# Kernel tuning notes

Measured on AMD Instinct MI355X. Metric: run time of the kernel, lower is better.

The kernel has to match this reference:

```python
import jax, jax.numpy as jnp
import numpy as np

NEG_SLOPE = 0.1
BN_EPS = 1e-5

def lrelu(z):
    return jax.nn.leaky_relu(z, NEG_SLOPE)

def conv1d(x, w, b):
    # x: [B,C,L], w: [O,I,K], 'same' padding for K=3
    y = jax.lax.conv_general_dilated(x, w, (1,), [(1, 1)], dimension_numbers=('NCH', 'OIH', 'NCH'))
    return y + b[None, :, None]

def batchnorm_train(x, g, be):
    # training-mode BatchNorm1d over (B, L) per channel; x: [B,C,L]
    m = x.mean(axis=(0, 2), keepdims=True)
    v = x.var(axis=(0, 2), keepdims=True)
    return g[None, :, None] * (x - m) * jax.lax.rsqrt(v + BN_EPS) + be[None, :, None]

def setup_inputs() -> dict:
    key = jax.random.key(0)
    ks = jax.random.split(key, 16)
    L, B, E = 100, 32, 512
    F, K, M, H, DEC = 256, 3, 128, 512, 512
    D = F + 2  # cnn feats + 2 coord dims
    s = 0.02
    inp = {
        'x': jax.random.normal(ks[0], (L, B, E), jnp.float32),
        'h': jax.random.normal(ks[1], (B, H), jnp.float32),
        'cw1': jax.random.normal(ks[2], (F, E, K), jnp.float32) * s,
        'cb1': jnp.zeros((F,), jnp.float32),
        'g1': jnp.ones((F,), jnp.float32), 'be1': jnp.zeros((F,), jnp.float32),
        'cw2': jax.random.normal(ks[3], (F, F, K), jnp.float32) * s,
        'cb2': jnp.zeros((F,), jnp.float32),
        'g2': jnp.ones((F,), jnp.float32), 'be2': jnp.zeros((F,), jnp.float32),
        'cw3': jax.random.normal(ks[4], (F, F, K), jnp.float32) * s,
        'cb3': jnp.zeros((F,), jnp.float32),
        'g3': jnp.ones((F,), jnp.float32), 'be3': jnp.zeros((F,), jnp.float32),
        'cw4': jax.random.normal(ks[5], (F, F, K), jnp.float32) * s,
        'cb4': jnp.zeros((F,), jnp.float32),
        'g4': jnp.ones((F,), jnp.float32), 'be4': jnp.zeros((F,), jnp.float32),
        'W1': jax.random.normal(ks[6], (2 * D + H, M), jnp.float32) * s,
        'b1': jnp.zeros((M,), jnp.float32),
        'W2': jax.random.normal(ks[7], (M, M), jnp.float32) * s,
        'b2': jnp.zeros((M,), jnp.float32),
        'W3': jax.random.normal(ks[8], (M, M), jnp.float32) * s,
        'b3': jnp.zeros((M,), jnp.float32),
        'W4': jax.random.normal(ks[9], (M, M), jnp.float32) * s,
        'b4': jnp.zeros((M,), jnp.float32),
        'F1': jax.random.normal(ks[10], (M, M), jnp.float32) * s,
        'fb1': jnp.zeros((M,), jnp.float32),
        'F2': jax.random.normal(ks[11], (M, DEC), jnp.float32) * s,
        'fb2': jnp.zeros((DEC,), jnp.float32),
    }
    return inp

def reference(x, h, cw1, cb1, g1, be1, cw2, cb2, g2, be2, cw3, cb3, g3, be3,
              cw4, cb4, g4, be4, W1, b1, W2, b2, W3, b3, W4, b4, F1, fb1, F2, fb2):
    # x: [L,B,E] -> [B,E,L]
    xc = jnp.transpose(x, (1, 2, 0))
    for cw, cb, g, be in ((cw1, cb1, g1, be1), (cw2, cb2, g2, be2),
                          (cw3, cb3, g3, be3), (cw4, cb4, g4, be4)):
        xc = batchnorm_train(lrelu(conv1d(xc, cw, cb)), g, be)
    xc = jnp.transpose(xc, (0, 2, 1))  # [B,L,F]
    B, L, _ = xc.shape
    # coordinate tensor: cvt_coord(i, L) = [(i/sqrt(L)-2)/2, (i%sqrt(L)-2)/2]
    i = jnp.arange(L, dtype=jnp.float32)
    sL = jnp.sqrt(jnp.float32(L))
    coord = jnp.stack([(i / sL - 2.0) / 2.0, (jnp.mod(i, sL) - 2.0) / 2.0], axis=-1)
    xf = jnp.concatenate([xc, jnp.broadcast_to(coord, (B, L, 2))], axis=-1)  # [B,L,D]
    D = xf.shape[-1]
    # pair[b,i,j] = [xf[b,j], xf[b,i], h[b]]; split W1 to avoid materializing concat
    Wa, Wb, Wc = W1[:D], W1[D:2 * D], W1[2 * D:]
    A = xf @ Wa                              # contribution of x_j, [B,L,M]
    C = xf @ Wb + (h @ Wc + b1)[:, None, :]  # contribution of x_i and h, [B,L,M]
    g = lrelu(C[:, :, None, :] + A[:, None, :, :])  # [B,L,L,M]
    g = lrelu(g @ W2 + b2)
    g = lrelu(g @ W3 + b3)
    g = lrelu(g @ W4 + b4)
    s = g.sum(axis=(1, 2))  # sum-pool over all L*L pairs -> [B,M]
    out = lrelu(lrelu(s @ F1 + fb1) @ F2 + fb2)  # [B,dec_hid]
    return out
```

## Files before the change

### kernel.cpp

```cpp
#include <hip/hip_runtime.h>
#include <hip/hip_bf16.h>
#include <stdint.h>
#include <stddef.h>

#define NEG 0.1f

typedef __attribute__((ext_vector_type(8))) short short8;
typedef __attribute__((ext_vector_type(16))) float floatx16;

__device__ __forceinline__ unsigned f2bf(float f) {
  union { float f; unsigned u; } v; v.f = f;
  unsigned r = v.u + 0x7FFFu + ((v.u >> 16) & 1u);
  return r >> 16;
}
__device__ __forceinline__ unsigned pk2bf(float a, float b) {
  __hip_bfloat162 h = __float22bfloat162_rn(make_float2(a, b));
  union { __hip_bfloat162 h; unsigned u; } v; v.h = h; return v.u;
}
__device__ __forceinline__ float bits2f(unsigned u) {
  union { unsigned u; float f; } v; v.u = u; return v.f;
}

__global__ void k_prep(const float* __restrict__ cw1, const float* __restrict__ cw2,
                       const float* __restrict__ cw3, const float* __restrict__ cw4,
                       unsigned short* __restrict__ wt1, unsigned short* __restrict__ wt2,
                       unsigned short* __restrict__ wt3, unsigned short* __restrict__ wt4,
                       const float* __restrict__ W1, unsigned short* __restrict__ wab,
                       const float* __restrict__ W2, const float* __restrict__ W3,
                       const float* __restrict__ W4, unsigned short* __restrict__ wmlp,
                       const float* __restrict__ h, float* __restrict__ hc) {
  __shared__ float tile[64 * 65];
  int bid = blockIdx.x, tid = threadIdx.x;
  if (bid < 1280) {
    int z = bid;
    int E; const float* cw; unsigned short* wt;
    if (z < 512) { E = 512; cw = cw1; wt = wt1; }
    else {
      int q = (z - 512) >> 8; E = 256;
      cw = (q == 0) ? cw2 : ((q == 1) ? cw3 : cw4);
      wt = (q == 0) ? wt2 : ((q == 1) ? wt3 : wt4);
      z = (z - 512) & 255;
    }
    int idx = z * 256 + tid;
    int f = idx / E, e = idx - f * E;
    const float* s = cw + (size_t)idx * 3;
    unsigned short* d = wt + (size_t)f * 3 * E + e;
    d[0] = (unsigned short)f2bf(s[0]);
    d[E] = (unsigned short)f2bf(s[1]);
    d[2 * E] = (unsigned short)f2bf(s[2]);
  } else if (bid < 1304) {
    int tw = bid - 1280;
    int half = tw / 12, rem = tw % 12, dt = rem >> 1, nt = rem & 1;
    int c = tid & 63, rq = tid >> 6;
#pragma unroll
    for (int it = 0; it < 16; ++it) {
      int r = rq + it * 4;
      int kp = dt * 64 + r;
      float v = 0.f;
      if (kp < 258) v = W1[(size_t)(half * 258 + kp) * 128 + nt * 64 + c];
      tile[r * 65 + c] = v;
    }
    __syncthreads();
#pragma unroll
    for (int it = 0; it < 16; ++it) {
      int r2 = rq + it * 4;
      wab[(size_t)(half * 128 + nt * 64 + r2) * 384 + dt * 64 + c] =
          (unsigned short)f2bf(tile[c * 65 + r2]);
    }
  } else if (bid < 1496) {
    int i2 = (bid - 1304) * 256 + tid;
    int n = i2 & 127, k = (i2 >> 7) & 127, zz = i2 >> 14;
    const float* W = (zz == 0) ? W2 : ((zz == 1) ? W3 : W4);
    float v = W[k * 128 + n];
    int w = n >> 5, l = ((k >> 3) & 1) * 32 + (n & 31), kk = k >> 4, j = k & 7;
    int i = (((zz * 4 + w) * 8 + kk) << 9) | (l << 3) | j;
    wmlp[i] = (unsigned short)f2bf(v);
  } else {
    int t = bid - 1496;
    int b = t >> 2, seg = t & 3;
    int m = tid & 127, sub = tid >> 7;
    int k0 = seg * 128 + sub * 64;
    const float* hr = h + b * 512 + k0;
    const float* Wc = W1 + (size_t)(516 + k0) * 128 + m;
    float a0 = 0.f, a1 = 0.f, a2 = 0.f, a3 = 0.f, a4 = 0.f, a5 = 0.f, a6 = 0.f, a7 = 0.f;
#pragma unroll
    for (int k = 0; k < 64; k += 8) {
      a0 += hr[k + 0] * Wc[(size_t)(k + 0) * 128];
      a1 += hr[k + 1] * Wc[(size_t)(k + 1) * 128];
      a2 += hr[k + 2] * Wc[(size_t)(k + 2) * 128];
      a3 += hr[k + 3] * Wc[(size_t)(k + 3) * 128];
      a4 += hr[k + 4] * Wc[(size_t)(k + 4) * 128];
      a5 += hr[k + 5] * Wc[(size_t)(k + 5) * 128];
      a6 += hr[k + 6] * Wc[(size_t)(k + 6) * 128];
      a7 += hr[k + 7] * Wc[(size_t)(k + 7) * 128];
    }
    float s = ((a0 + a1) + (a2 + a3)) + ((a4 + a5) + (a6 + a7));
    atomicAdd(&hc[b * 128 + m], s);
  }
}

__global__ __launch_bounds__(128, 2) void k_conv(
    const float* __restrict__ zin, const float* __restrict__ bnin,
    const float* __restrict__ gamv, const float* __restrict__ betv,
    const unsigned short* __restrict__ wt, const float* __restrict__ cb,
    float* __restrict__ zout, float* __restrict__ bnout, int E, int xmode) {
  extern __shared__ unsigned short smem[];
  const int SL = (E == 512) ? 520 : 264;
  unsigned short* slab = smem;
  unsigned short* Bs = smem + 34 * SL;
  const int K = 3 * E, NC = K >> 6;
  const int esh = (E == 512) ? 9 : 8;
  int tid = threadIdx.x;
  int lane = tid & 63, wave = tid >> 6;
  int r0 = blockIdx.x * 32, ct = blockIdx.y;
  int i32 = lane & 31;
  int koff = (lane >> 5) << 3;

  int lrow = (r0 + i32) % 100;
  bool vks0 = (lrow >= 1), vks2 = (lrow <= 98);

  if (xmode) {
    for (int s = wave; s < 34; s += 2) {
      int m = r0 - 1 + s; m = min(max(m, 0), 3199);
      int b = m / 100, l = m - b * 100;
      size_t base = (size_t)(l * 32 + b) * 512;
#pragma unroll
      for (int cc = 0; cc < 2; ++cc) {
        int ch = cc * 256 + lane * 4;
        float4 v = *(const float4*)(zin + base + ch);
        uint2 p; p.x = pk2bf(v.x, v.y); p.y = pk2bf(v.z, v.w);
        *(uint2*)(&slab[s * SL + ch]) = p;
      }
    }
  } else {
    const float inv = 1.f / 3200.f;
    float sc[4], sh[4];
#pragma unroll
    for (int q = 0; q < 4; ++q) {
      int ch = lane * 4 + q;
      float mme = bnin[ch] * inv;
      float var = bnin[256 + ch] * inv - mme * mme;
      sc[q] = gamv[ch] * rsqrtf(var + 1e-5f);
      sh[q] = betv[ch] - mme * sc[q];
    }
    for (int s = wave; s < 34; s += 2) {
      int m = r0 - 1 + s; m = min(max(m, 0), 3199);
      float4 v = *(const float4*)(zin + (size_t)m * 256 + lane * 4);
      uint2 p;
      p.x = pk2bf(v.x * sc[0] + sh[0], v.y * sc[1] + sh[1]);
      p.y = pk2bf(v.z * sc[2] + sh[2], v.w * sc[3] + sh[3]);
      *(uint2*)(&slab[s * SL + lane * 4]) = p;
    }
  }

  floatx16 acc;
#pragma unroll
  for (int q = 0; q < 16; ++q) acc[q] = 0.f;

  int brow = tid >> 1, bhalf = (tid & 1) * 32;
  uint4 pre[4];
#pragma unroll
  for (int t = 0; t < 4; ++t)
    pre[t] = *(const uint4*)(wt + (size_t)(ct * 64 + brow) * K + bhalf + t * 8);

  for (int c = 0; c < NC; ++c) {
    unsigned short* Bc = Bs + (c & 1) * (64 * 72);
#pragma unroll
    for (int t = 0; t < 4; ++t)
      *(uint4*)(&Bc[brow * 72 + bhalf + t * 8]) = pre[t];
    __syncthreads();
    if (c + 1 < NC) {
#pragma unroll
      for (int t = 0; t < 4; ++t)
        pre[t] = *(const uint4*)(wt + (size_t)(ct * 64 + brow) * K + (c + 1) * 64 + bhalf + t * 8);
    }
    int ks = (c << 6) >> esh;
    int ebase = (c << 6) & (E - 1);
    bool v = (ks == 0) ? vks0 : ((ks == 2) ? vks2 : true);
    int srow = i32 + ks;
#pragma unroll
    for (int kk = 0; kk < 4; ++kk) {
      short8 a = {};
      if (v) a = *(const short8*)(&slab[srow * SL + ebase + kk * 16 + koff]);
      short8 b8 = *(const short8*)(&Bc[(wave * 32 + i32) * 72 + kk * 16 + koff]);
      acc = __builtin_amdgcn_mfma_f32_32x32x16_bf16(a, b8, acc, 0, 0, 0);
    }
  }

  int f = ct * 64 + wave * 32 + i32;
  float bias = cb[f];
  float s1 = 0.f, s2 = 0.f;
#pragma unroll
  for (int reg = 0; reg < 16; ++reg) {
    int rowp = (reg & 3) + 8 * (reg >> 2) + 4 * (lane >> 5);
    int m = r0 + rowp;
    float v = acc[reg] + bias;
    v = fmaxf(v, NEG * v);
    zout[(size_t)m * 256 + f] = v;
    s1 += v; s2 += v * v;
  }
  s1 += __shfl_xor(s1, 32, 64);
  s2 += __shfl_xor(s2, 32, 64);
  if (lane < 32) { atomicAdd(&bnout[f], s1); atomicAdd(&bnout[256 + f], s2); }
}

__global__ __launch_bounds__(128, 2) void k_ac(
    const float* __restrict__ zin, const float* __restrict__ bnin,
    const float* __restrict__ gamv, const float* __restrict__ betv,
    const unsigned short* __restrict__ wab, const float* __restrict__ hc,
    const float* __restrict__ b1v,
    unsigned short* __restrict__ Abf, unsigned short* __restrict__ Cbf) {
  __shared__ unsigned short slab[32 * 328];
  __shared__ unsigned short Bs[2 * 64 * 72];
  int tid = threadIdx.x;
  int lane = tid & 63, wave = tid >> 6;
  int r0 = blockIdx.x * 32, ct = blockIdx.y;
  int i32 = lane & 31;
  int koff = (lane >> 5) << 3;
  const float inv = 1.f / 3200.f;

  {
    float sc[4], sh[4];
#pragma unroll
    for (int q = 0; q < 4; ++q) {
      int ch = lane * 4 + q;
      float mme = bnin[ch] * inv;
      float var = bnin[256 + ch] * inv - mme * mme;
      sc[q] = gamv[ch] * rsqrtf(var + 1e-5f);
      sh[q] = betv[ch] - mme * sc[q];
    }
    for (int s = wave; s < 32; s += 2) {
      int m = r0 + s;
      float4 v = *(const float4*)(zin + (size_t)m * 256 + lane * 4);
      uint2 p;
      p.x = pk2bf(v.x * sc[0] + sh[0], v.y * sc[1] + sh[1]);
      p.y = pk2bf(v.z * sc[2] + sh[2], v.w * sc[3] + sh[3]);
      *(uint2*)(&slab[s * 328 + lane * 4]) = p;
    }
    if (wave == 0) {
      int s = i32, half = (lane >> 5) * 32;
      int m = r0 + s, l = m % 100;
      float c0 = ((float)l * 0.1f - 2.0f) * 0.5f;
      float c1 = ((float)(l % 10) - 2.0f) * 0.5f;
#pragma unroll
      for (int seg = 0; seg < 4; ++seg) {
        uint4 z4; z4.x = z4.y = z4.z = z4.w = 0u;
        if (half == 0 && seg == 0) z4.x = pk2bf(c0, c1);
        *(uint4*)(&slab[s * 328 + 256 + half + seg * 8]) = z4;
      }
    }
  }

  floatx16 acc;
#pragma unroll
  for (int q = 0; q < 16; ++q) acc[q] = 0.f;

  int brow = tid >> 1, bhalf = (tid & 1) * 32;
  uint4 pre[4];
#pragma unroll
  for (int t = 0; t < 4; ++t)
    pre[t] = *(const uint4*)(wab + (size_t)(ct * 64 + brow) * 384 + bhalf + t * 8);

  for (int c = 0; c < 5; ++c) {
    unsigned short* Bc = Bs + (c & 1) * (64 * 72);
#pragma unroll
    for (int t = 0; t < 4; ++t)
      *(uint4*)(&Bc[brow * 72 + bhalf + t * 8]) = pre[t];
    __syncthreads();
    if (c + 1 < 5) {
#pragma unroll
      for (int t = 0; t < 4; ++t)
        pre[t] = *(const uint4*)(wab + (size_t)(ct * 64 + brow) * 384 + (c + 1) * 64 + bhalf + t * 8);
    }
#pragma unroll
    for (int kk = 0; kk < 4; ++kk) {
      short8 a = *(const short8*)(&slab[i32 * 328 + c * 64 + kk * 16 + koff]);
      short8 b8 = *(const short8*)(&Bc[(wave * 32 + i32) * 72 + kk * 16 + koff]);
      acc = __builtin_amdgcn_mfma_f32_32x32x16_bf16(a, b8, acc, 0, 0, 0);
    }
  }

  int n = ct * 64 + wave * 32 + i32;
#pragma unroll
  for (int reg = 0; reg < 16; ++reg) {
    int rowp = (reg & 3) + 8 * (reg >> 2) + 4 * (lane >> 5);
    int m = r0 + rowp;
    float v = acc[reg];
    if (ct < 2) {
      Abf[(size_t)m * 128 + n] = (unsigned short)f2bf(v);
    } else {
      int b = m / 100;
      int nc = n - 128;
      Cbf[(size_t)m * 128 + nc] =
          (unsigned short)f2bf(v + hc[b * 128 + nc] + b1v[nc]);
    }
  }
}

__global__ __launch_bounds__(256, 2) void k_mlp(
    const unsigned short* __restrict__ Abf, const unsigned short* __restrict__ Cbf,
    const unsigned short* __restrict__ wmlp, const float* __restrict__ b2,
    const float* __restrict__ b3, const float* __restrict__ b4,
    float* __restrict__ sout) {
  __shared__ unsigned short gs0[128 * 136];
  __shared__ unsigned short gs1[128 * 136];
  int tid = threadIdx.x, lane = tid & 63, wave = tid >> 6;
  int ln31 = lane & 31;
  int half = lane >> 5;
  int koff = half << 3;
  int wb = wave * 32;

  short8 wreg[3][8];
#pragma unroll
  for (int z = 0; z < 3; ++z)
#pragma unroll
    for (int kk = 0; kk < 8; ++kk)
      wreg[z][kk] = *(const short8*)(wmlp + (size_t)(((z * 4 + wave) * 8 + kk) * 512) + lane * 8);

  float4 bq[2][4];
#pragma unroll
  for (int q = 0; q < 4; ++q) {
    bq[0][q] = *(const float4*)(b2 + wb + q * 8 + 4 * half);
    bq[1][q] = *(const float4*)(b3 + wb + q * 8 + 4 * half);
  }
  float bv4 = b4[wb + ln31];

  for (int ti = 0; ti < 2; ++ti) {
    int t = blockIdx.x + ti * 1264;
    int b = t / 79, tt = t - b * 79;
    __syncthreads();
    {
      int lr = wb + (lane >> 1);
      int hh = lane & 1;
      int r = tt * 128 + lr;
      if (r > 9999) r = 9999;
      const unsigned short* Crow = Cbf + (size_t)(b * 100 + r / 100) * 128;
      const unsigned short* Arow = Abf + (size_t)(b * 100 + r % 100) * 128;
#pragma unroll
      for (int it = 0; it < 8; ++it) {
        int cc = hh * 64 + it * 8;
        uint4 c4 = *(const uint4*)(Crow + cc);
        uint4 a4 = *(const uint4*)(Arow + cc);
        unsigned cw[4] = {c4.x, c4.y, c4.z, c4.w};
        unsigned aw[4] = {a4.x, a4.y, a4.z, a4.w};
        unsigned ow[4];
#pragma unroll
        for (int q = 0; q < 4; ++q) {
          float x0 = bits2f(cw[q] << 16) + bits2f(aw[q] << 16);
          float x1 = bits2f(cw[q] & 0xFFFF0000u) + bits2f(aw[q] & 0xFFFF0000u);
          x0 = fmaxf(x0, NEG * x0);
          x1 = fmaxf(x1, NEG * x1);
          ow[q] = pk2bf(x0, x1);
        }
        uint4 o4; o4.x = ow[0]; o4.y = ow[1]; o4.z = ow[2]; o4.w = ow[3];
        *(uint4*)(&gs0[lr * 136 + cc]) = o4;
      }
    }
    __syncthreads();

#pragma unroll
    for (int z = 0; z < 2; ++z) {
      const unsigned short* src = z ? gs1 : gs0;
      unsigned short* dst = z ? gs0 : gs1;
#pragma unroll
      for (int rg = 0; rg < 4; ++rg) {
        floatx16 acc;
#pragma unroll
        for (int q = 0; q < 16; ++q) acc[q] = 0.f;
#pragma unroll
        for (int kk = 0; kk < 8; ++kk) {
          short8 g8 = *(const short8*)(&src[(rg * 32 + ln31) * 136 + kk * 16 + koff]);
          acc = __builtin_amdgcn_mfma_f32_32x32x16_bf16(wreg[z][kk], g8, acc, 0, 0, 0);
        }
        int pr = rg * 32 + ln31;
#pragma unroll
        for (int q = 0; q < 4; ++q) {
          float4 bb = bq[z][q];
          float v0 = acc[q * 4 + 0] + bb.x; v0 = fmaxf(v0, NEG * v0);
          float v1 = acc[q * 4 + 1] + bb.y; v1 = fmaxf(v1, NEG * v1);
          float v2 = acc[q * 4 + 2] + bb.z; v2 = fmaxf(v2, NEG * v2);
          float v3 = acc[q * 4 + 3] + bb.w; v3 = fmaxf(v3, NEG * v3);
          uint2 p; p.x = pk2bf(v0, v1); p.y = pk2bf(v2, v3);
          *(uint2*)(&dst[pr * 136 + wb + q * 8 + 4 * half]) = p;
        }
      }
      __syncthreads();
    }

    float colsum = 0.f;
#pragma unroll
    for (int rg = 0; rg < 4; ++rg) {
      floatx16 acc;
#pragma unroll
      for (int q = 0; q < 16; ++q) acc[q] = 0.f;
#pragma unroll
      for (int kk = 0; kk < 8; ++kk) {
        short8 a8 = *(const short8*)(&gs0[(rg * 32 + ln31) * 136 + kk * 16 + koff]);
        acc = __builtin_amdgcn_mfma_f32_32x32x16_bf16(a8, wreg[2][kk], acc, 0, 0, 0);
      }
#pragma unroll
      for (int reg = 0; reg < 16; ++reg) {
        int rowp = (reg & 3) + 8 * (reg >> 2) + 4 * half;
        int p = tt * 128 + rg * 32 + rowp;
        float v = acc[reg] + bv4;
        v = fmaxf(v, NEG * v);
        colsum += (p < 10000) ? v : 0.f;
      }
    }
    colsum += __shfl_xor(colsum, 32, 64);
    if (lane < 32) atomicAdd(&sout[b * 128 + wb + lane], colsum);
  }
}

__global__ void k_final(const float* __restrict__ s, const float* __restrict__ F1,
                        const float* __restrict__ fb1, const float* __restrict__ F2,
                        const float* __restrict__ fb2, float* __restrict__ out) {
  __shared__ float sl[128], t1[128];
  int b = blockIdx.x, t = threadIdx.x;
  if (t < 128) sl[t] = s[b * 128 + t];
  __syncthreads();
  if (t < 128) {
    float a = fb1[t];
    for (int k = 0; k < 128; ++k) a += sl[k] * F1[k * 128 + t];
    t1[t] = fmaxf(a, NEG * a);
  }
  __syncthreads();
  for (int o = t; o < 512; o += 256) {
    float a = fb2[o];
    for (int k = 0; k < 128; ++k) a += t1[k] * F2[k * 512 + o];
    out[b * 512 + o] = fmaxf(a, NEG * a);
  }
}

extern "C" void kernel_launch(void* const* d_in, const int* in_sizes, int n_in,
                              void* d_out, int out_size, void* d_ws, size_t ws_size,
                              hipStream_t stream) {
  const float* x   = (const float*)d_in[0];
  const float* h   = (const float*)d_in[1];
  const float* cw1 = (const float*)d_in[2];
  const float* cb1 = (const float*)d_in[3];
  const float* g1  = (const float*)d_in[4];
  const float* be1 = (const float*)d_in[5];
  const float* cw2 = (const float*)d_in[6];
  const float* cb2 = (const float*)d_in[7];
  const float* g2  = (const float*)d_in[8];
  const float* be2 = (const float*)d_in[9];
  const float* cw3 = (const float*)d_in[10];
  const float* cb3 = (const float*)d_in[11];
  const float* g3  = (const float*)d_in[12];
  const float* be3 = (const float*)d_in[13];
  const float* cw4 = (const float*)d_in[14];
  const float* cb4 = (const float*)d_in[15];
  const float* g4  = (const float*)d_in[16];
  const float* be4 = (const float*)d_in[17];
  const float* W1  = (const float*)d_in[18];
  const float* b1  = (const float*)d_in[19];
  const float* W2  = (const float*)d_in[20];
  const float* b2  = (const float*)d_in[21];
  const float* W3  = (const float*)d_in[22];
  const float* b3  = (const float*)d_in[23];
  const float* W4  = (const float*)d_in[24];
  const float* b4  = (const float*)d_in[25];
  const float* F1  = (const float*)d_in[26];
  const float* fb1 = (const float*)d_in[27];
  const float* F2  = (const float*)d_in[28];
  const float* fb2 = (const float*)d_in[29];

  char* ws = (char*)d_ws;
  float* bn0  = (float*)(ws + 0);
  float* bn1  = (float*)(ws + 2048);
  float* bn2  = (float*)(ws + 4096);
  float* bn3  = (float*)(ws + 6144);
  float* sbuf = (float*)(ws + 8192);
  float* hc   = (float*)(ws + 24576);
  float* za   = (float*)(ws + 40960);
  float* zb   = (float*)(ws + 3317760);
  unsigned short* wt1  = (unsigned short*)(ws + 6594560);
  unsigned short* wt2  = (unsigned short*)(ws + 7380992);
  unsigned short* wt3  = (unsigned short*)(ws + 7774208);
  unsigned short* wt4  = (unsigned short*)(ws + 8167424);
  unsigned short* wab  = (unsigned short*)(ws + 8560640);
  unsigned short* wmlp = (unsigned short*)(ws + 8757248);
  unsigned short* Abf  = (unsigned short*)(ws + 8855552);
  unsigned short* Cbf  = (unsigned short*)(ws + 9674752);

  hipMemsetAsync(d_ws, 0, 40960, stream);

  k_prep<<<1624, 256, 0, stream>>>(cw1, cw2, cw3, cw4, wt1, wt2, wt3, wt4,
                                   W1, wab, W2, W3, W4, wmlp, h, hc);

  const int lds1 = (34 * 520 + 2 * 64 * 72) * 2;
  const int lds2 = (34 * 264 + 2 * 64 * 72) * 2;
  k_conv<<<dim3(100, 4), 128, lds1, stream>>>(x,  nullptr, nullptr, nullptr, wt1, cb1, za, bn0, 512, 1);
  k_conv<<<dim3(100, 4), 128, lds2, stream>>>(za, bn0, g1, be1, wt2, cb2, zb, bn1, 256, 0);
  k_conv<<<dim3(100, 4), 128, lds2, stream>>>(zb, bn1, g2, be2, wt3, cb3, za, bn2, 256, 0);
  k_conv<<<dim3(100, 4), 128, lds2, stream>>>(za, bn2, g3, be3, wt4, cb4, zb, bn3, 256, 0);

  k_ac<<<dim3(100, 4), 128, 0, stream>>>(zb, bn3, g4, be4, wab, hc, b1, Abf, Cbf);

  k_mlp<<<1264, 256, 0, stream>>>(Abf, Cbf, wmlp, b2, b3, b4, sbuf);
  k_final<<<32, 256, 0, stream>>>(sbuf, F1, fb1, F2, fb2, (float*)d_out);
}
```

Baseline: 292.3 us.

## Fuse prep, conv and A/C stages into one persistent kernel with grid barriers

Merges the weight-prep kernel, the four conv+BN kernels and the A/C projection kernel into a single persistent kernel of 400 blocks that synchronises through atomic-counter grid barriers instead of separate launches. This is meant to remove per-launch overhead and tail gaps between the small dependent stages. It relies on all 400 blocks being co-resident, since a spin barrier deadlocks otherwise, and it forces the largest static LDS footprint onto every phase. Separately, the MLP kernel's LDS tiles drop the row padding and use an XOR swizzle to avoid bank conflicts while using less shared memory.

```diff
diff --git a/kernel.cpp b/kernel.cpp
--- a/kernel.cpp
+++ b/kernel.cpp
@@ -4,6 +4,7 @@
 #include <stddef.h>
 
 #define NEG 0.1f
+#define NB 400
 
 typedef __attribute__((ext_vector_type(8))) short short8;
 typedef __attribute__((ext_vector_type(16))) float floatx16;
@@ -14,105 +15,38 @@
   return r >> 16;
 }
 __device__ __forceinline__ unsigned pk2bf(float a, float b) {
-  __hip_bfloat162 h = __float22bfloat162_rn(make_float2(a, b));
-  union { __hip_bfloat162 h; unsigned u; } v; v.h = h; return v.u;
+  __hip_bfloat162 hh = __float22bfloat162_rn(make_float2(a, b));
+  union { __hip_bfloat162 h; unsigned u; } v; v.h = hh; return v.u;
 }
 __device__ __forceinline__ float bits2f(unsigned u) {
   union { unsigned u; float f; } v; v.u = u; return v.f;
 }
 
-__global__ void k_prep(const float* __restrict__ cw1, const float* __restrict__ cw2,
-                       const float* __restrict__ cw3, const float* __restrict__ cw4,
-                       unsigned short* __restrict__ wt1, unsigned short* __restrict__ wt2,
-                       unsigned short* __restrict__ wt3, unsigned short* __restrict__ wt4,
-                       const float* __restrict__ W1, unsigned short* __restrict__ wab,
-                       const float* __restrict__ W2, const float* __restrict__ W3,
-                       const float* __restrict__ W4, unsigned short* __restrict__ wmlp,
-                       const float* __restrict__ h, float* __restrict__ hc) {
-  __shared__ float tile[64 * 65];
-  int bid = blockIdx.x, tid = threadIdx.x;
-  if (bid < 1280) {
-    int z = bid;
-    int E; const float* cw; unsigned short* wt;
-    if (z < 512) { E = 512; cw = cw1; wt = wt1; }
-    else {
-      int q = (z - 512) >> 8; E = 256;
-      cw = (q == 0) ? cw2 : ((q == 1) ? cw3 : cw4);
-      wt = (q == 0) ? wt2 : ((q == 1) ? wt3 : wt4);
-      z = (z - 512) & 255;
-    }
-    int idx = z * 256 + tid;
-    int f = idx / E, e = idx - f * E;
-    const float* s = cw + (size_t)idx * 3;
-    unsigned short* d = wt + (size_t)f * 3 * E + e;
-    d[0] = (unsigned short)f2bf(s[0]);
-    d[E] = (unsigned short)f2bf(s[1]);
-    d[2 * E] = (unsigned short)f2bf(s[2]);
-  } else if (bid < 1304) {
-    int tw = bid - 1280;
-    int half = tw / 12, rem = tw % 12, dt = rem >> 1, nt = rem & 1;
-    int c = tid & 63, rq = tid >> 6;
-#pragma unroll
-    for (int it = 0; it < 16; ++it) {
-      int r = rq + it * 4;
-      int kp = dt * 64 + r;
-      float v = 0.f;
-      if (kp < 258) v = W1[(size_t)(half * 258 + kp) * 128 + nt * 64 + c];
-      tile[r * 65 + c] = v;
-    }
-    __syncthreads();
-#pragma unroll
-    for (int it = 0; it < 16; ++it) {
-      int r2 = rq + it * 4;
-      wab[(size_t)(half * 128 + nt * 64 + r2) * 384 + dt * 64 + c] =
-          (unsigned short)f2bf(tile[c * 65 + r2]);
-    }
-  } else if (bid < 1496) {
-    int i2 = (bid - 1304) * 256 + tid;
-    int n = i2 & 127, k = (i2 >> 7) & 127, zz = i2 >> 14;
-    const float* W = (zz == 0) ? W2 : ((zz == 1) ? W3 : W4);
-    float v = W[k * 128 + n];
-    int w = n >> 5, l = ((k >> 3) & 1) * 32 + (n & 31), kk = k >> 4, j = k & 7;
-    int i = (((zz * 4 + w) * 8 + kk) << 9) | (l << 3) | j;
-    wmlp[i] = (unsigned short)f2bf(v);
-  } else {
-    int t = bid - 1496;
-    int b = t >> 2, seg = t & 3;
-    int m = tid & 127, sub = tid >> 7;
-    int k0 = seg * 128 + sub * 64;
-    const float* hr = h + b * 512 + k0;
-    const float* Wc = W1 + (size_t)(516 + k0) * 128 + m;
-    float a0 = 0.f, a1 = 0.f, a2 = 0.f, a3 = 0.f, a4 = 0.f, a5 = 0.f, a6 = 0.f, a7 = 0.f;
-#pragma unroll
-    for (int k = 0; k < 64; k += 8) {
-      a0 += hr[k + 0] * Wc[(size_t)(k + 0) * 128];
-      a1 += hr[k + 1] * Wc[(size_t)(k + 1) * 128];
-      a2 += hr[k + 2] * Wc[(size_t)(k + 2) * 128];
-      a3 += hr[k + 3] * Wc[(size_t)(k + 3) * 128];
-      a4 += hr[k + 4] * Wc[(size_t)(k + 4) * 128];
-      a5 += hr[k + 5] * Wc[(size_t)(k + 5) * 128];
-      a6 += hr[k + 6] * Wc[(size_t)(k + 6) * 128];
-      a7 += hr[k + 7] * Wc[(size_t)(k + 7) * 128];
-    }
-    float s = ((a0 + a1) + (a2 + a3)) + ((a4 + a5) + (a6 + a7));
-    atomicAdd(&hc[b * 128 + m], s);
-  }
-}
-
-__global__ __launch_bounds__(128, 2) void k_conv(
+__device__ __forceinline__ void gridbar(unsigned* cnt, int phase) {
+  __syncthreads();
+  if (threadIdx.x == 0) {
+    __threadfence();
+    __hip_atomic_fetch_add(cnt + phase, 1u, __ATOMIC_ACQ_REL, __HIP_MEMORY_SCOPE_AGENT);
+    while (__hip_atomic_load(cnt + phase, __ATOMIC_ACQUIRE, __HIP_MEMORY_SCOPE_AGENT) < NB)
+      __builtin_amdgcn_s_sleep(1);
+  }
+  __syncthreads();
+  __threadfence();
+}
+
+__device__ __forceinline__ void conv_phase(
     const float* __restrict__ zin, const float* __restrict__ bnin,
     const float* __restrict__ gamv, const float* __restrict__ betv,
     const unsigned short* __restrict__ wt, const float* __restrict__ cb,
-    float* __restrict__ zout, float* __restrict__ bnout, int E, int xmode) {
-  extern __shared__ unsigned short smem[];
+    float* __restrict__ zout, float* __restrict__ bnout, int E, int xmode,
+    unsigned short* smem, int rt, int ct, int tid) {
   const int SL = (E == 512) ? 520 : 264;
   unsigned short* slab = smem;
   unsigned short* Bs = smem + 34 * SL;
   const int K = 3 * E, NC = K >> 6;
   const int esh = (E == 512) ? 9 : 8;
-  int tid = threadIdx.x;
   int lane = tid & 63, wave = tid >> 6;
-  int r0 = blockIdx.x * 32, ct = blockIdx.y;
+  int r0 = rt * 32;
   int i32 = lane & 31;
   int koff = (lane >> 5) << 3;
 
@@ -204,17 +138,17 @@
   if (lane < 32) { atomicAdd(&bnout[f], s1); atomicAdd(&bnout[256 + f], s2); }
 }
 
-__global__ __launch_bounds__(128, 2) void k_ac(
+__device__ __forceinline__ void ac_phase(
     const float* __restrict__ zin, const float* __restrict__ bnin,
     const float* __restrict__ gamv, const float* __restrict__ betv,
     const unsigned short* __restrict__ wab, const float* __restrict__ hc,
     const float* __restrict__ b1v,
-    unsigned short* __restrict__ Abf, unsigned short* __restrict__ Cbf) {
-  __shared__ unsigned short slab[32 * 328];
-  __shared__ unsigned short Bs[2 * 64 * 72];
-  int tid = threadIdx.x;
+    unsigned short* __restrict__ Abf, unsigned short* __restrict__ Cbf,
+    unsigned short* smem, int rt, int ct, int tid) {
+  unsigned short* slab = smem;
+  unsigned short* Bs = smem + 32 * 328;
   int lane = tid & 63, wave = tid >> 6;
-  int r0 = blockIdx.x * 32, ct = blockIdx.y;
+  int r0 = rt * 32;
   int i32 = lane & 31;
   int koff = (lane >> 5) << 3;
   const float inv = 1.f / 3200.f;
@@ -297,18 +231,120 @@
   }
 }
 
+__global__ __launch_bounds__(128, 2) void k_chain(
+    const float* __restrict__ x, const float* __restrict__ h,
+    const float* __restrict__ cw1, const float* __restrict__ cb1,
+    const float* __restrict__ g1, const float* __restrict__ be1,
+    const float* __restrict__ cw2, const float* __restrict__ cb2,
+    const float* __restrict__ g2, const float* __restrict__ be2,
+    const float* __restrict__ cw3, const float* __restrict__ cb3,
+    const float* __restrict__ g3, const float* __restrict__ be3,
+    const float* __restrict__ cw4, const float* __restrict__ cb4,
+    const float* __restrict__ g4, const float* __restrict__ be4,
+    const float* __restrict__ W1, const float* __restrict__ b1,
+    const float* __restrict__ W2, const float* __restrict__ W3,
+    const float* __restrict__ W4,
+    unsigned short* __restrict__ wt1, unsigned short* __restrict__ wt2,
+    unsigned short* __restrict__ wt3, unsigned short* __restrict__ wt4,
+    unsigned short* __restrict__ wab, unsigned short* __restrict__ wmlp,
+    float* __restrict__ hc, unsigned* __restrict__ cnt,
+    float* __restrict__ za, float* __restrict__ zb,
+    float* __restrict__ bn0, float* __restrict__ bn1,
+    float* __restrict__ bn2, float* __restrict__ bn3,
+    unsigned short* __restrict__ Abf, unsigned short* __restrict__ Cbf) {
+  __shared__ unsigned short smem[34 * 520 + 2 * 64 * 72];
+  int tid = threadIdx.x, bx = blockIdx.x;
+  int gtid = bx * 128 + tid;
+
+  for (int i = gtid; i < 327680; i += 51200) {
+    const float* cw; unsigned short* wt; int E, esh, idx;
+    if (i < 131072) { cw = cw1; wt = wt1; E = 512; esh = 9; idx = i; }
+    else {
+      int j = i - 131072; int q = j >> 16; idx = j & 65535; E = 256; esh = 8;
+      cw = (q == 0) ? cw2 : ((q == 1) ? cw3 : cw4);
+      wt = (q == 0) ? wt2 : ((q == 1) ? wt3 : wt4);
+    }
+    int f = idx >> esh, e = idx & (E - 1);
+    const float* s = cw + (size_t)idx * 3;
+    unsigned short* d = wt + (size_t)f * 3 * E + e;
+    d[0] = (unsigned short)f2bf(s[0]);
+    d[E] = (unsigned short)f2bf(s[1]);
+    d[2 * E] = (unsigned short)f2bf(s[2]);
+  }
+  if (gtid < 49152) {
+    int n = gtid & 127, k = (gtid >> 7) & 127, zz = gtid >> 14;
+    const float* W = (zz == 0) ? W2 : ((zz == 1) ? W3 : W4);
+    float v = W[k * 128 + n];
+    int w = n >> 5, l = ((k >> 3) & 1) * 32 + (n & 31), kk = k >> 4, j = k & 7;
+    int i = (((zz * 4 + w) * 8 + kk) << 9) | (l << 3) | j;
+    wmlp[i] = (unsigned short)f2bf(v);
+  }
+  if (bx >= 24 && bx < 280) {
+    int t = bx - 24;
+    int b = t >> 3, seg = t & 7;
+    int k0 = seg * 64;
+    const float* hr = h + b * 512 + k0;
+    const float* Wc = W1 + (size_t)(516 + k0) * 128 + tid;
+    float a0 = 0.f, a1 = 0.f, a2 = 0.f, a3 = 0.f, a4 = 0.f, a5 = 0.f, a6 = 0.f, a7 = 0.f;
+#pragma unroll
+    for (int k = 0; k < 64; k += 8) {
+      a0 += hr[k + 0] * Wc[(size_t)(k + 0) * 128];
+      a1 += hr[k + 1] * Wc[(size_t)(k + 1) * 128];
+      a2 += hr[k + 2] * Wc[(size_t)(k + 2) * 128];
+      a3 += hr[k + 3] * Wc[(size_t)(k + 3) * 128];
+      a4 += hr[k + 4] * Wc[(size_t)(k + 4) * 128];
+      a5 += hr[k + 5] * Wc[(size_t)(k + 5) * 128];
+      a6 += hr[k + 6] * Wc[(size_t)(k + 6) * 128];
+      a7 += hr[k + 7] * Wc[(size_t)(k + 7) * 128];
+    }
+    float s = ((a0 + a1) + (a2 + a3)) + ((a4 + a5) + (a6 + a7));
+    atomicAdd(&hc[b * 128 + tid], s);
+  }
+  if (bx < 24) {
+    float* tile = (float*)smem;
+    int half = bx / 12, rem = bx % 12, dt = rem >> 1, nt = rem & 1;
+    int c = tid & 63, rq = tid >> 6;
+#pragma unroll
+    for (int it = 0; it < 32; ++it) {
+      int r = rq + it * 2;
+      int kp = dt * 64 + r;
+      float v = 0.f;
+      if (kp < 258) v = W1[(size_t)(half * 258 + kp) * 128 + nt * 64 + c];
+      tile[r * 65 + c] = v;
+    }
+    __syncthreads();
+#pragma unroll
+    for (int it = 0; it < 32; ++it) {
+      int r2 = rq + it * 2;
+      wab[(size_t)(half * 128 + nt * 64 + r2) * 384 + dt * 64 + c] =
+          (unsigned short)f2bf(tile[c * 65 + r2]);
+    }
+  }
+  gridbar(cnt, 0);
+
+  int rt = bx % 100, ct = bx / 100;
+  conv_phase(x, 0, 0, 0, wt1, cb1, za, bn0, 512, 1, smem, rt, ct, tid);
+  gridbar(cnt, 1);
+  conv_phase(za, bn0, g1, be1, wt2, cb2, zb, bn1, 256, 0, smem, rt, ct, tid);
+  gridbar(cnt, 2);
+  conv_phase(zb, bn1, g2, be2, wt3, cb3, za, bn2, 256, 0, smem, rt, ct, tid);
+  gridbar(cnt, 3);
+  conv_phase(za, bn2, g3, be3, wt4, cb4, zb, bn3, 256, 0, smem, rt, ct, tid);
+  gridbar(cnt, 4);
+  ac_phase(zb, bn3, g4, be4, wab, hc, b1, Abf, Cbf, smem, rt, ct, tid);
+}
+
 __global__ __launch_bounds__(256, 2) void k_mlp(
     const unsigned short* __restrict__ Abf, const unsigned short* __restrict__ Cbf,
     const unsigned short* __restrict__ wmlp, const float* __restrict__ b2,
     const float* __restrict__ b3, const float* __restrict__ b4,
     float* __restrict__ sout) {
-  __shared__ unsigned short gs0[128 * 136];
-  __shared__ unsigned short gs1[128 * 136];
+  __shared__ unsigned short gs0[128 * 128];
+  __shared__ unsigned short gs1[128 * 128];
   int tid = threadIdx.x, lane = tid & 63, wave = tid >> 6;
   int ln31 = lane & 31;
   int half = lane >> 5;
-  int koff = half << 3;
-  int wb = wave * 32;
+  int rx = ln31 & 15;
 
   short8 wreg[3][8];
 #pragma unroll
@@ -317,6 +353,7 @@
     for (int kk = 0; kk < 8; ++kk)
       wreg[z][kk] = *(const short8*)(wmlp + (size_t)(((z * 4 + wave) * 8 + kk) * 512) + lane * 8);
 
+  int wb = wave * 32;
   float4 bq[2][4];
 #pragma unroll
   for (int q = 0; q < 4; ++q) {
@@ -332,6 +369,7 @@
     {
       int lr = wb + (lane >> 1);
       int hh = lane & 1;
+      int lbase = lr * 128, lrx = lr & 15;
       int r = tt * 128 + lr;
       if (r > 9999) r = 9999;
       const unsigned short* Crow = Cbf + (size_t)(b * 100 + r / 100) * 128;
@@ -353,7 +391,7 @@
           ow[q] = pk2bf(x0, x1);
         }
         uint4 o4; o4.x = ow[0]; o4.y = ow[1]; o4.z = ow[2]; o4.w = ow[3];
-        *(uint4*)(&gs0[lr * 136 + cc]) = o4;
+        *(uint4*)(&gs0[lbase + (((hh * 8 + it) ^ lrx) << 3)]) = o4;
       }
     }
     __syncthreads();
@@ -367,12 +405,14 @@
         floatx16 acc;
 #pragma unroll
         for (int q = 0; q < 16; ++q) acc[q] = 0.f;
+        int rowb = (rg * 32 + ln31) * 128;
 #pragma unroll
         for (int kk = 0; kk < 8; ++kk) {
-          short8 g8 = *(const short8*)(&src[(rg * 32 + ln31) * 136 + kk * 16 + koff]);
+          short8 g8 = *(const short8*)(&src[rowb + (((kk * 2 + half) ^ rx) << 3)]);
           acc = __builtin_amdgcn_mfma_f32_32x32x16_bf16(wreg[z][kk], g8, acc, 0, 0, 0);
         }
         int pr = rg * 32 + ln31;
+        int prb = pr * 128;
 #pragma unroll
         for (int q = 0; q < 4; ++q) {
           float4 bb = bq[z][q];
@@ -381,7 +421,7 @@
           float v2 = acc[q * 4 + 2] + bb.z; v2 = fmaxf(v2, NEG * v2);
           float v3 = acc[q * 4 + 3] + bb.w; v3 = fmaxf(v3, NEG * v3);
           uint2 p; p.x = pk2bf(v0, v1); p.y = pk2bf(v2, v3);
-          *(uint2*)(&dst[pr * 136 + wb + q * 8 + 4 * half]) = p;
+          *(uint2*)(&dst[prb + (((wave * 4 + q) ^ rx) << 3) + half * 4]) = p;
         }
       }
       __syncthreads();
@@ -393,9 +433,10 @@
       floatx16 acc;
 #pragma unroll
       for (int q = 0; q < 16; ++q) acc[q] = 0.f;
+      int rowb = (rg * 32 + ln31) * 128;
 #pragma unroll
       for (int kk = 0; kk < 8; ++kk) {
-        short8 a8 = *(const short8*)(&gs0[(rg * 32 + ln31) * 136 + kk * 16 + koff]);
+        short8 a8 = *(const short8*)(&gs0[rowb + (((kk * 2 + half) ^ rx) << 3)]);
         acc = __builtin_amdgcn_mfma_f32_32x32x16_bf16(a8, wreg[2][kk], acc, 0, 0, 0);
       }
 #pragma unroll
@@ -473,30 +514,25 @@
   float* bn3  = (float*)(ws + 6144);
   float* sbuf = (float*)(ws + 8192);
   float* hc   = (float*)(ws + 24576);
-  float* za   = (float*)(ws + 40960);
-  float* zb   = (float*)(ws + 3317760);
-  unsigned short* wt1  = (unsigned short*)(ws + 6594560);
-  unsigned short* wt2  = (unsigned short*)(ws + 7380992);
-  unsigned short* wt3  = (unsigned short*)(ws + 7774208);
-  unsigned short* wt4  = (unsigned short*)(ws + 8167424);
-  unsigned short* wab  = (unsigned short*)(ws + 8560640);
-  unsigned short* wmlp = (unsigned short*)(ws + 8757248);
-  unsigned short* Abf  = (unsigned short*)(ws + 8855552);
-  unsigned short* Cbf  = (unsigned short*)(ws + 9674752);
-
-  hipMemsetAsync(d_ws, 0, 40960, stream);
-
-  k_prep<<<1624, 256, 0, stream>>>(cw1, cw2, cw3, cw4, wt1, wt2, wt3, wt4,
-                                   W1, wab, W2, W3, W4, wmlp, h, hc);
-
-  const int lds1 = (34 * 520 + 2 * 64 * 72) * 2;
-  const int lds2 = (34 * 264 + 2 * 64 * 72) * 2;
-  k_conv<<<dim3(100, 4), 128, lds1, stream>>>(x,  nullptr, nullptr, nullptr, wt1, cb1, za, bn0, 512, 1);
-  k_conv<<<dim3(100, 4), 128, lds2, stream>>>(za, bn0, g1, be1, wt2, cb2, zb, bn1, 256, 0);
-  k_conv<<<dim3(100, 4), 128, lds2, stream>>>(zb, bn1, g2, be2, wt3, cb3, za, bn2, 256, 0);
-  k_conv<<<dim3(100, 4), 128, lds2, stream>>>(za, bn2, g3, be3, wt4, cb4, zb, bn3, 256, 0);
-
-  k_ac<<<dim3(100, 4), 128, 0, stream>>>(zb, bn3, g4, be4, wab, hc, b1, Abf, Cbf);
+  unsigned* cnt = (unsigned*)(ws + 40960);
+  float* za   = (float*)(ws + 49152);
+  float* zb   = (float*)(ws + 3325952);
+  unsigned short* wt1  = (unsigned short*)(ws + 6602752);
+  unsigned short* wt2  = (unsigned short*)(ws + 7389184);
+  unsigned short* wt3  = (unsigned short*)(ws + 7782400);
+  unsigned short* wt4  = (unsigned short*)(ws + 8175616);
+  unsigned short* wab  = (unsigned short*)(ws + 8568832);
+  unsigned short* wmlp = (unsigned short*)(ws + 8765440);
+  unsigned short* Abf  = (unsigned short*)(ws + 8863744);
+  unsigned short* Cbf  = (unsigned short*)(ws + 9682944);
+
+  hipMemsetAsync(d_ws, 0, 41024, stream);
+
+  k_chain<<<NB, 128, 0, stream>>>(
+      x, h, cw1, cb1, g1, be1, cw2, cb2, g2, be2, cw3, cb3, g3, be3,
+      cw4, cb4, g4, be4, W1, b1, W2, W3, W4,
+      wt1, wt2, wt3, wt4, wab, wmlp, hc, cnt,
+      za, zb, bn0, bn1, bn2, bn3, Abf, Cbf);
 
   k_mlp<<<1264, 256, 0, stream>>>(Abf, Cbf, wmlp, b2, b3, b4, sbuf);
   k_final<<<32, 256, 0, stream>>>(sbuf, F1, fb1, F2, fb2, (float*)d_out);
```

Measured after the change: 589.3 us. 102% more time.

## Split conv K-loop across wave pairs and XOR-swizzle MLP LDS tiles

Applied to the files above, without the earlier changes.

The conv kernel now runs 256 threads per block. Two wave pairs each handle half of the reduction chunks and combine their partial accumulators through shared memory before the bias, activation and BN statistics step. This doubles the waves working on the serial K-loop for the same 400-block grid, at the cost of an extra reduction pass and more LDS. Separately, the MLP kernel drops the padded 136-stride LDS tiles in favour of unpadded 128-stride tiles with XOR-swizzled 16-byte chunks, which cuts LDS use and is meant to avoid bank conflicts.

```diff
diff --git a/kernel.cpp b/kernel.cpp
--- a/kernel.cpp
+++ b/kernel.cpp
@@ -14,8 +14,8 @@
   return r >> 16;
 }
 __device__ __forceinline__ unsigned pk2bf(float a, float b) {
-  __hip_bfloat162 h = __float22bfloat162_rn(make_float2(a, b));
-  union { __hip_bfloat162 h; unsigned u; } v; v.h = h; return v.u;
+  __hip_bfloat162 hh = __float22bfloat162_rn(make_float2(a, b));
+  union { __hip_bfloat162 h; unsigned u; } v; v.h = hh; return v.u;
 }
 __device__ __forceinline__ float bits2f(unsigned u) {
   union { unsigned u; float f; } v; v.u = u; return v.f;
@@ -99,7 +99,7 @@
   }
 }
 
-__global__ __launch_bounds__(128, 2) void k_conv(
+__global__ __launch_bounds__(256, 2) void k_conv(
     const float* __restrict__ zin, const float* __restrict__ bnin,
     const float* __restrict__ gamv, const float* __restrict__ betv,
     const unsigned short* __restrict__ wt, const float* __restrict__ cb,
@@ -108,10 +108,11 @@
   const int SL = (E == 512) ? 520 : 264;
   unsigned short* slab = smem;
   unsigned short* Bs = smem + 34 * SL;
-  const int K = 3 * E, NC = K >> 6;
+  const int K = 3 * E, NC = K >> 6, NCH = NC >> 1;
   const int esh = (E == 512) ? 9 : 8;
   int tid = threadIdx.x;
   int lane = tid & 63, wave = tid >> 6;
+  int khalf = wave >> 1, cwave = wave & 1;
   int r0 = blockIdx.x * 32, ct = blockIdx.y;
   int i32 = lane & 31;
   int koff = (lane >> 5) << 3;
@@ -120,7 +121,7 @@
   bool vks0 = (lrow >= 1), vks2 = (lrow <= 98);
 
   if (xmode) {
-    for (int s = wave; s < 34; s += 2) {
+    for (int s = wave; s < 34; s += 4) {
       int m = r0 - 1 + s; m = min(max(m, 0), 3199);
       int b = m / 100, l = m - b * 100;
       size_t base = (size_t)(l * 32 + b) * 512;
@@ -143,7 +144,7 @@
       sc[q] = gamv[ch] * rsqrtf(var + 1e-5f);
       sh[q] = betv[ch] - mme * sc[q];
     }
-    for (int s = wave; s < 34; s += 2) {
+    for (int s = wave; s < 34; s += 4) {
       int m = r0 - 1 + s; m = min(max(m, 0), 3199);
       float4 v = *(const float4*)(zin + (size_t)m * 256 + lane * 4);
       uint2 p;
@@ -157,51 +158,65 @@
 #pragma unroll
   for (int q = 0; q < 16; ++q) acc[q] = 0.f;
 
-  int brow = tid >> 1, bhalf = (tid & 1) * 32;
+  int t128 = tid & 127;
+  int brow = t128 >> 1, bhalf = (t128 & 1) * 32;
+  const unsigned short* wrow = wt + (size_t)(ct * 64 + brow) * K + khalf * NCH * 64 + bhalf;
   uint4 pre[4];
 #pragma unroll
-  for (int t = 0; t < 4; ++t)
-    pre[t] = *(const uint4*)(wt + (size_t)(ct * 64 + brow) * K + bhalf + t * 8);
-
-  for (int c = 0; c < NC; ++c) {
-    unsigned short* Bc = Bs + (c & 1) * (64 * 72);
+  for (int t = 0; t < 4; ++t) pre[t] = *(const uint4*)(wrow + t * 8);
+
+  for (int c = 0; c < NCH; ++c) {
+    unsigned short* Bc = Bs + (khalf * 2 + (c & 1)) * (64 * 72);
 #pragma unroll
     for (int t = 0; t < 4; ++t)
       *(uint4*)(&Bc[brow * 72 + bhalf + t * 8]) = pre[t];
     __syncthreads();
-    if (c + 1 < NC) {
+    if (c + 1 < NCH) {
 #pragma unroll
       for (int t = 0; t < 4; ++t)
-        pre[t] = *(const uint4*)(wt + (size_t)(ct * 64 + brow) * K + (c + 1) * 64 + bhalf + t * 8);
-    }
-    int ks = (c << 6) >> esh;
-    int ebase = (c << 6) & (E - 1);
+        pre[t] = *(const uint4*)(wrow + (c + 1) * 64 + t * 8);
+    }
+    int cg = khalf * NCH + c;
+    int ks = (cg << 6) >> esh;
+    int ebase = (cg << 6) & (E - 1);
     bool v = (ks == 0) ? vks0 : ((ks == 2) ? vks2 : true);
     int srow = i32 + ks;
 #pragma unroll
     for (int kk = 0; kk < 4; ++kk) {
       short8 a = {};
       if (v) a = *(const short8*)(&slab[srow * SL + ebase + kk * 16 + koff]);
-      short8 b8 = *(const short8*)(&Bc[(wave * 32 + i32) * 72 + kk * 16 + koff]);
+      short8 b8 = *(const short8*)(&Bc[(cwave * 32 + i32) * 72 + kk * 16 + koff]);
       acc = __builtin_amdgcn_mfma_f32_32x32x16_bf16(a, b8, acc, 0, 0, 0);
     }
   }
 
-  int f = ct * 64 + wave * 32 + i32;
-  float bias = cb[f];
-  float s1 = 0.f, s2 = 0.f;
-#pragma unroll
-  for (int reg = 0; reg < 16; ++reg) {
-    int rowp = (reg & 3) + 8 * (reg >> 2) + 4 * (lane >> 5);
-    int m = r0 + rowp;
-    float v = acc[reg] + bias;
-    v = fmaxf(v, NEG * v);
-    zout[(size_t)m * 256 + f] = v;
-    s1 += v; s2 += v * v;
-  }
-  s1 += __shfl_xor(s1, 32, 64);
-  s2 += __shfl_xor(s2, 32, 64);
-  if (lane < 32) { atomicAdd(&bnout[f], s1); atomicAdd(&bnout[256 + f], s2); }
+  __syncthreads();
+  float* scr = (float*)smem;
+  if (khalf == 1) {
+#pragma unroll
+    for (int reg = 0; reg < 16; ++reg) {
+      int rowp = (reg & 3) + 8 * (reg >> 2) + 4 * (lane >> 5);
+      scr[cwave * 1024 + rowp * 32 + i32] = acc[reg];
+    }
+  }
+  __syncthreads();
+  if (khalf == 0) {
+    int f = ct * 64 + cwave * 32 + i32;
+    float bias = cb[f];
+    float s1 = 0.f, s2 = 0.f;
+#pragma unroll
+    for (int reg = 0; reg < 16; ++reg) {
+      int rowp = (reg & 3) + 8 * (reg >> 2) + 4 * (lane >> 5);
+      int m = r0 + rowp;
+      float v = acc[reg] + scr[cwave * 1024 + rowp * 32 + i32] + bias;
+      v = fmaxf(v, NEG * v);
+      zout[(size_t)m * 256 + f] = v;
+      s1 += v; s2 += v * v;
+    }
+    s1 += __shfl_xor(s1, 32, 64);
+    s2 += __shfl_xor(s2, 32, 64);
+    if (lane < 32) { atomicAdd(&bnout[f], s1); atomicAdd(&bnout[256 + f], s2); }
+  }
 }
 
 __global__ __launch_bounds__(128, 2) void k_ac(
@@ -302,13 +317,12 @@
     const unsigned short* __restrict__ wmlp, const float* __restrict__ b2,
     const float* __restrict__ b3, const float* __restrict__ b4,
     float* __restrict__ sout) {
-  __shared__ unsigned short gs0[128 * 136];
-  __shared__ unsigned short gs1[128 * 136];
+  __shared__ unsigned short gs0[128 * 128];
+  __shared__ unsigned short gs1[128 * 128];
   int tid = threadIdx.x, lane = tid & 63, wave = tid >> 6;
   int ln31 = lane & 31;
   int half = lane >> 5;
-  int koff = half << 3;
-  int wb = wave * 32;
+  int rx = ln31 & 15;
 
   short8 wreg[3][8];
 #pragma unroll
@@ -317,6 +331,7 @@
     for (int kk = 0; kk < 8; ++kk)
       wreg[z][kk] = *(const short8*)(wmlp + (size_t)(((z * 4 + wave) * 8 + kk) * 512) + lane * 8);
 
+  int wb = wave * 32;
   float4 bq[2][4];
 #pragma unroll
   for (int q = 0; q < 4; ++q) {
@@ -332,6 +347,7 @@
     {
       int lr = wb + (lane >> 1);
       int hh = lane & 1;
+      int lbase = lr * 128, lrx = lr & 15;
       int r = tt * 128 + lr;
       if (r > 9999) r = 9999;
       const unsigned short* Crow = Cbf + (size_t)(b * 100 + r / 100) * 128;
@@ -353,7 +369,7 @@
           ow[q] = pk2bf(x0, x1);
         }
         uint4 o4; o4.x = ow[0]; o4.y = ow[1]; o4.z = ow[2]; o4.w = ow[3];
-        *(uint4*)(&gs0[lr * 136 + cc]) = o4;
+        *(uint4*)(&gs0[lbase + (((hh * 8 + it) ^ lrx) << 3)]) = o4;
       }
     }
     __syncthreads();
@@ -367,12 +383,14 @@
         floatx16 acc;
 #pragma unroll
         for (int q = 0; q < 16; ++q) acc[q] = 0.f;
+        int rowb = (rg * 32 + ln31) * 128;
 #pragma unroll
         for (int kk = 0; kk < 8; ++kk) {
-          short8 g8 = *(const short8*)(&src[(rg * 32 + ln31) * 136 + kk * 16 + koff]);
+          short8 g8 = *(const short8*)(&src[rowb + (((kk * 2 + half) ^ rx) << 3)]);
           acc = __builtin_amdgcn_mfma_f32_32x32x16_bf16(wreg[z][kk], g8, acc, 0, 0, 0);
         }
         int pr = rg * 32 + ln31;
+        int prb = pr * 128;
 #pragma unroll
         for (int q = 0; q < 4; ++q) {
           float4 bb = bq[z][q];
@@ -381,7 +399,7 @@
           float v2 = acc[q * 4 + 2] + bb.z; v2 = fmaxf(v2, NEG * v2);
           float v3 = acc[q * 4 + 3] + bb.w; v3 = fmaxf(v3, NEG * v3);
           uint2 p; p.x = pk2bf(v0, v1); p.y = pk2bf(v2, v3);
-          *(uint2*)(&dst[pr * 136 + wb + q * 8 + 4 * half]) = p;
+          *(uint2*)(&dst[prb + (((wave * 4 + q) ^ rx) << 3) + half * 4]) = p;
         }
       }
       __syncthreads();
@@ -393,9 +411,10 @@
       floatx16 acc;
 #pragma unroll
       for (int q = 0; q < 16; ++q) acc[q] = 0.f;
+      int rowb = (rg * 32 + ln31) * 128;
 #pragma unroll
       for (int kk = 0; kk < 8; ++kk) {
-        short8 a8 = *(const short8*)(&gs0[(rg * 32 + ln31) * 136 + kk * 16 + koff]);
+        short8 a8 = *(const short8*)(&gs0[rowb + (((kk * 2 + half) ^ rx) << 3)]);
         acc = __builtin_amdgcn_mfma_f32_32x32x16_bf16(a8, wreg[2][kk], acc, 0, 0, 0);
       }
 #pragma unroll
@@ -489,12 +508,12 @@
   k_prep<<<1624, 256, 0, stream>>>(cw1, cw2, cw3, cw4, wt1, wt2, wt3, wt4,
                                    W1, wab, W2, W3, W4, wmlp, h, hc);
 
-  const int lds1 = (34 * 520 + 2 * 64 * 72) * 2;
-  const int lds2 = (34 * 264 + 2 * 64 * 72) * 2;
-  k_conv<<<dim3(100, 4), 128, lds1, stream>>>(x,  nullptr, nullptr, nullptr, wt1, cb1, za, bn0, 512, 1);
-  k_conv<<<dim3(100, 4), 128, lds2, stream>>>(za, bn0, g1, be1, wt2, cb2, zb, bn1, 256, 0);
-  k_conv<<<dim3(100, 4), 128, lds2, stream>>>(zb, bn1, g2, be2, wt3, cb3, za, bn2, 256, 0);
-  k_conv<<<dim3(100, 4), 128, lds2, stream>>>(za, bn2, g3, be3, wt4, cb4, zb, bn3, 256, 0);
+  const int lds1 = (34 * 520 + 4 * 64 * 72) * 2;
+  const int lds2 = (34 * 264 + 4 * 64 * 72) * 2;
+  k_conv<<<dim3(100, 4), 256, lds1, stream>>>(x,  nullptr, nullptr, nullptr, wt1, cb1, za, bn0, 512, 1);
+  k_conv<<<dim3(100, 4), 256, lds2, stream>>>(za, bn0, g1, be1, wt2, cb2, zb, bn1, 256, 0);
+  k_conv<<<dim3(100, 4), 256, lds2, stream>>>(zb, bn1, g2, be2, wt3, cb3, za, bn2, 256, 0);
+  k_conv<<<dim3(100, 4), 256, lds2, stream>>>(za, bn2, g3, be3, wt4, cb4, zb, bn3, 256, 0);
 
   k_ac<<<dim3(100, 4), 128, 0, stream>>>(zb, bn3, g4, be4, wab, hc, b1, Abf, Cbf);
 
```

Measured after the change: 283.6 us. 1.03x faster.
